# Optimization experiments

Measured on AMD Instinct MI355X. Metric: run time of the kernel, lower is better.

The kernel has to match this reference:

```python
import jax, jax.numpy as jnp
import numpy as np

B, T, I, H, O = 128, 256, 64, 1024, 64


def setup_inputs() -> dict:
    key = jax.random.key(0)
    ks = jax.random.split(key, 16)
    s_ih1 = 1.0 / np.sqrt(H)
    def mk(k, shape, s):
        return jax.random.uniform(k, shape, jnp.float32, -s, s)
    return {
        "x": jax.random.normal(ks[0], (B, T, I), jnp.float32),
        # RNNCell 1: input I -> hidden H
        "W_ih1": mk(ks[1], (H, I), s_ih1),
        "b_ih1": mk(ks[2], (H,), s_ih1),
        "W_hh1": mk(ks[3], (H, H), s_ih1),
        "b_hh1": mk(ks[4], (H,), s_ih1),
        # RNNCell 2: hidden H -> hidden H
        "W_ih2": mk(ks[5], (H, H), s_ih1),
        "b_ih2": mk(ks[6], (H,), s_ih1),
        "W_hh2": mk(ks[7], (H, H), s_ih1),
        "b_hh2": mk(ks[8], (H,), s_ih1),
        # gate: 2H -> H
        "Wg": mk(ks[9], (H, 2 * H), 1.0 / np.sqrt(2 * H)),
        "bg": mk(ks[10], (H,), 1.0 / np.sqrt(2 * H)),
        # output heads: H -> O
        "Wo1": mk(ks[11], (O, H), s_ih1),
        "bo1": mk(ks[12], (O,), s_ih1),
        "Wo2": mk(ks[13], (O, H), s_ih1),
        "bo2": mk(ks[14], (O,), s_ih1),
    }


def reference(x, W_ih1, b_ih1, W_hh1, b_hh1, W_ih2, b_ih2, W_hh2, b_hh2,
              Wg, bg, Wo1, bo1, Wo2, bo2):
    batch = x.shape[0]
    h1_0 = jnp.zeros((batch, H), x.dtype)
    h2_0 = jnp.zeros((batch, H), x.dtype)
    u_0 = jnp.ones((batch, H), x.dtype)

    def step(carry, x_t):
        h1, h2, u = carry
        # RNNCell 1
        h1 = jnp.tanh(x_t @ W_ih1.T + b_ih1 + h1 @ W_hh1.T + b_hh1)
        # RNNCell 2, gated convex blend with previous h2
        h2_new = jnp.tanh(h1 @ W_ih2.T + b_ih2 + h2 @ W_hh2.T + b_hh2)
        h2 = u * h2_new + (1.0 - u) * h2
        # dual tanh output head
        out = jnp.tanh(h1 @ Wo1.T + bo1) + jnp.tanh(h2 @ Wo2.T + bo2)
        # gate for NEXT step, computed from current hiddens
        u = jax.nn.sigmoid(jnp.concatenate([h1, h2], axis=1) @ Wg.T + bg)
        return (h1, h2, u), out

    xs = jnp.swapaxes(x, 0, 1)  # [T, B, I]
    _, outs = jax.lax.scan(step, (h1_0, h2_0, u_0), xs)
    return jnp.swapaxes(outs, 0, 1)  # [B, T, O]
```

## Files before the change

### kernel.cpp

```cpp
#include <hip/hip_runtime.h>
#include <cstddef>

using bf16x8 = __attribute__((ext_vector_type(8))) short;
using f32x4  = __attribute__((ext_vector_type(4))) float;

constexpr int Bb = 128;
constexpr int Tt = 256;
constexpr int Hh = 1024;
constexpr int Oo = 64;
constexpr int NBLK = 200;
constexpr int FLAG_STRIDE = 32;
constexpr int RS = 1048;

constexpr int R_H1 = 8;
constexpr int R_H2 = 16;
constexpr int R_PP = 6;
constexpr int R_PO = 16;

constexpr int FH1 = 0;
constexpr int FP2 = 64;
constexpr int FPG = 96;
constexpr int FPO = 128;
constexpr int FH2 = 160;
constexpr int FZO = 224;

__device__ __forceinline__ float bf2f(short s) {
  unsigned int u = ((unsigned int)(unsigned short)s) << 16;
  float f;
  __builtin_memcpy(&f, &u, 4);
  return f;
}
__device__ __forceinline__ short f2bf(float f) {
  unsigned int u;
  __builtin_memcpy(&u, &f, 4);
  u += 0x7fffu + ((u >> 16) & 1u);
  return (short)(u >> 16);
}
__device__ __forceinline__ bf16x8 as_bf(int4 v) {
  union { int4 i; bf16x8 b; } u; u.i = v; return u.b;
}
__device__ __forceinline__ float ldf(const float* p) {
  return __hip_atomic_load((float*)p, __ATOMIC_RELAXED, __HIP_MEMORY_SCOPE_AGENT);
}
__device__ __forceinline__ void stf(float* p, float v) {
  __hip_atomic_store(p, v, __ATOMIC_RELAXED, __HIP_MEMORY_SCOPE_AGENT);
}
__device__ __forceinline__ unsigned ldu(const unsigned* p) {
  return __hip_atomic_load((unsigned*)p, __ATOMIC_RELAXED, __HIP_MEMORY_SCOPE_AGENT);
}

#define LD16A(d, p) asm volatile("global_load_dwordx4 %0, %1, off sc1" \
                                 : "=v"(d) : "v"((const void*)(p)))

__device__ __forceinline__ void stage_chunk(short* dstAs, const short* src, int tid) {
  const int row = tid >> 3;
  const int c0  = (tid & 7) * 8;
  const short* gp = src + (size_t)row * Hh + c0;
  short* lp = dstAs + row * RS + c0;
  int4 r0[16];
#pragma unroll
  for (int j = 0; j < 16; ++j) LD16A(r0[j], gp + j * 64);
  asm volatile("s_waitcnt vmcnt(0)" ::: "memory");
#pragma unroll
  for (int j = 0; j < 16; ++j) *(int4*)(lp + j * 64) = r0[j];
}

__device__ __forceinline__ void loadW(int4 (&w)[32], const short* B, size_t st,
                                      int lm, int q) {
  const short* bp = B + (size_t)lm * st + q * 8;
#pragma unroll
  for (int c = 0; c < 32; ++c) w[c] = *(const int4*)(bp + c * 32);
}

__device__ __forceinline__ void passW2(const short* As32, int lm, int q,
    const int4 (&w)[32], f32x4& acc0, f32x4& acc1) {
  const short* ap0 = As32 + lm * RS + q * 8;
  const short* ap1 = ap0 + 16 * RS;
#pragma unroll
  for (int c = 0; c < 32; ++c) {
    const bf16x8 a0 = as_bf(*(const int4*)(ap0 + c * 32));
    const bf16x8 a1 = as_bf(*(const int4*)(ap1 + c * 32));
    const bf16x8 b  = as_bf(w[c]);
    acc0 = __builtin_amdgcn_mfma_f32_16x16x32_bf16(a0, b, acc0, 0, 0, 0);
    acc1 = __builtin_amdgcn_mfma_f32_16x16x32_bf16(a1, b, acc1, 0, 0, 0);
  }
}

__device__ __forceinline__ void poll_ge(const unsigned* flags, int base,
                                        int mask, unsigned gen) {
  const unsigned* f = flags + (size_t)(base + (threadIdx.x & mask)) * FLAG_STRIDE;
  while (!__all(ldu(f) >= gen))
    __builtin_amdgcn_s_sleep(2);
}

#define POST_FLAG(SLOT, GEN) do {                                          \
    asm volatile("s_waitcnt vmcnt(0) lgkmcnt(0)" ::: "memory");            \
    __syncthreads();                                                       \
    if (tid == 0)                                                          \
      __hip_atomic_store(p.flags + (size_t)(SLOT) * FLAG_STRIDE,           \
                         (unsigned)(GEN),                                  \
                         __ATOMIC_RELAXED, __HIP_MEMORY_SCOPE_AGENT);      \
  } while (0)

#define ST_BF16_PAIR(BASE, ROW, COL, HV) do {                              \
    const int _ov = __shfl_xor((int)(unsigned short)(HV), 1, 64);          \
    if ((lm & 1) == 0) {                                                   \
      const unsigned _pk = (unsigned)(unsigned short)(HV) | ((unsigned)_ov << 16); \
      __hip_atomic_store((unsigned*)((BASE) + (size_t)(ROW) * Hh + (COL)), _pk, \
                         __ATOMIC_RELAXED, __HIP_MEMORY_SCOPE_AGENT);      \
    } } while (0)

struct RP {
  short *h1ring;
  short *h2ring;
  float *h2f;
  float *pre2f;
  float *pg1f;
  float *po1f;
  const short* prex;
  const short *whh1, *wih2, *whh2, *wg, *wo1, *wo2;
  const float *b_ih2, *b_hh2, *bg, *bo1, *bo2;
  float* out;
  unsigned* flags;
};

__global__ void __launch_bounds__(256, 1) rnn_kernel(RP p) {
  __shared__ short As[64 * RS];
  __shared__ float zbuf[2048];
  const int tid = threadIdx.x;
  const int lane = tid & 63;
  const int wv = tid >> 6;
  const int lm = lane & 15;
  const int q = lane >> 4;
  const int bid = blockIdx.x;

  const size_t HS = (size_t)Bb * Hh;
  const f32x4 z4 = {0.f, 0.f, 0.f, 0.f};
  int4 w[32];

  if (bid < 64) {
    const int g = bid;
    const int mb = (g >> 4) * 32, cb = (g & 15) * 64;
    const int cw = cb + wv * 16;
    loadW(w, p.whh1 + (size_t)cw * Hh, Hh, lm, q);
    for (int t = 0; t < Tt; ++t) {
      short prs[2][4];
      const short* pr = p.prex + (size_t)t * HS;
#pragma unroll
      for (int rf = 0; rf < 2; ++rf)
#pragma unroll
        for (int r = 0; r < 4; ++r)
          prs[rf][r] = pr[(size_t)(mb + rf * 16 + q * 4 + r) * Hh + cw + lm];
      if (tid < 64) {
        if (t >= 1) poll_ge(p.flags, FH1, 63, (unsigned)t);
        if (t >= 8) {
          poll_ge(p.flags, FP2, 31, (unsigned)(t - 7));
          poll_ge(p.flags, FPG, 31, (unsigned)(t - 7));
          poll_ge(p.flags, FPO, 3,  (unsigned)(t - 7));
        }
      }
      __syncthreads();
      const short* h1prev = p.h1ring + (size_t)((t + R_H1 - 1) % R_H1) * HS;
      stage_chunk(As, h1prev + (size_t)mb * Hh, tid);
      __syncthreads();
      f32x4 a0 = z4, a1 = z4;
      passW2(As, lm, q, w, a0, a1);
      short* h1out = p.h1ring + (size_t)(t % R_H1) * HS;
#pragma unroll
      for (int rf = 0; rf < 2; ++rf)
#pragma unroll
        for (int r = 0; r < 4; ++r) {
          const int row = mb + rf * 16 + q * 4 + r;
          const float z = rf ? a1[r] : a0[r];
          const short hv = f2bf(tanhf(z + bf2f(prs[rf][r])));
          ST_BF16_PAIR(h1out, row, cw + lm, hv);
        }
      POST_FLAG(FH1 + g, t + 1);
    }
  } else if (bid < 128) {
    const bool isP2 = (bid < 96);
    const int g = isP2 ? (bid - 64) : (bid - 96);
    const int mb = (g >> 4) * 64, cb = (g & 15) * 64;
    const int cw = cb + wv * 16;
    float bias;
    if (isP2) {
      bias = p.b_ih2[cw + lm] + p.b_hh2[cw + lm];
      loadW(w, p.wih2 + (size_t)cw * Hh, Hh, lm, q);
    } else {
      bias = p.bg[cw + lm];
      loadW(w, p.wg + (size_t)cw * (2 * Hh), 2 * Hh, lm, q);
    }
    const int fbase = isP2 ? FP2 : FPG;
    const int fslot = fbase + g;
    for (int t = 0; t < Tt; ++t) {
      if (tid < 64) {
        poll_ge(p.flags, FH1, 63, (unsigned)(t + 1));
        if (t >= R_PP) poll_ge(p.flags, FH2, 63, (unsigned)(t - (isP2 ? 5 : 4)));
      }
      __syncthreads();
      const short* h1cur = p.h1ring + (size_t)(t % R_H1) * HS;
      stage_chunk(As, h1cur + (size_t)mb * Hh, tid);
      stage_chunk(As + 32 * RS, h1cur + (size_t)(mb + 32) * Hh, tid);
      __syncthreads();
      f32x4 acc[4];
      acc[0] = acc[1] = acc[2] = acc[3] = (f32x4){bias, bias, bias, bias};
      passW2(As, lm, q, w, acc[0], acc[1]);
      passW2(As + 32 * RS, lm, q, w, acc[2], acc[3]);
      float* dst = (isP2 ? p.pre2f : p.pg1f) + (size_t)(t % R_PP) * HS;
#pragma unroll
      for (int rf = 0; rf < 4; ++rf)
#pragma unroll
        for (int r = 0; r < 4; ++r) {
          const int row = mb + rf * 16 + q * 4 + r;
          stf(dst + (size_t)row * Hh + cw + lm, acc[rf][r]);
        }
      POST_FLAG(fslot, t + 1);
    }
  } else if (bid < 192) {
    const int g = bid - 128;
    const int mb = (g >> 5) * 64, cb = (g & 31) * 32;
    const int m = wv >> 1;
    const int ch = wv & 1;
    const int cw = cb + ch * 16;
    if (m == 0) loadW(w, p.whh2 + (size_t)cw * Hh, Hh, lm, q);
    else        loadW(w, p.wg + Hh + (size_t)cw * (2 * Hh), 2 * Hh, lm, q);
    for (int s = 0; s < Tt; ++s) {
      if (tid < 64) {
        poll_ge(p.flags, FP2, 31, (unsigned)(s + 1));
        if (s >= 1) {
          poll_ge(p.flags, FPG, 31, (unsigned)s);
          poll_ge(p.flags, FH2, 63, (unsigned)s);
        }
        if (s >= R_H2) poll_ge(p.flags, FZO, 3, (unsigned)(s - 15));
      }
      __syncthreads();
      float p2v[4][4], pg1v[4][4], hpv[4][4];
      if (m == 0) {
        const float* pre2s = p.pre2f + (size_t)(s % R_PP) * HS;
        const float* pg1s  = p.pg1f + (size_t)((s + R_PP - 1) % R_PP) * HS;
#pragma unroll
        for (int rf = 0; rf < 4; ++rf)
#pragma unroll
          for (int r = 0; r < 4; ++r) {
            const size_t idx = (size_t)(mb + rf * 16 + q * 4 + r) * Hh + cw + lm;
            p2v[rf][r] = ldf(pre2s + idx);
            pg1v[rf][r] = (s > 0) ? ldf(pg1s + idx) : 0.f;
            hpv[rf][r] = p.h2f[idx];
          }
      }
      const short* h2prev = p.h2ring + (size_t)((s + R_H2 - 1) % R_H2) * HS;
      stage_chunk(As, h2prev + (size_t)mb * Hh, tid);
      stage_chunk(As + 32 * RS, h2prev + (size_t)(mb + 32) * Hh, tid);
      __syncthreads();
      f32x4 acc[4];
      acc[0] = acc[1] = acc[2] = acc[3] = z4;
      passW2(As, lm, q, w, acc[0], acc[1]);
      passW2(As + 32 * RS, lm, q, w, acc[2], acc[3]);
      if (m == 1) {
        float* zb = zbuf + ch * 1024;
#pragma unroll
        for (int rf = 0; rf < 4; ++rf)
#pragma unroll
          for (int r = 0; r < 4; ++r)
            zb[(rf * 4 + r) * 64 + lane] = acc[rf][r];
      }
      __syncthreads();
      if (m == 0) {
        const float* zb = zbuf + ch * 1024;
        short* h2out = p.h2ring + (size_t)(s % R_H2) * HS;
#pragma unroll
        for (int rf = 0; rf < 4; ++rf)
#pragma unroll
          for (int r = 0; r < 4; ++r) {
            const int row = mb + rf * 16 + q * 4 + r;
            const size_t idx = (size_t)row * Hh + cw + lm;
            const float zg = zb[(rf * 4 + r) * 64 + lane];
            const float u = (s == 0) ? 1.f
                : 1.f / (1.f + expf(-(zg + pg1v[rf][r])));
            const float hn = tanhf(acc[rf][r] + p2v[rf][r]);
            const float nv = fmaf(u, hn - hpv[rf][r], hpv[rf][r]);
            p.h2f[idx] = nv;
            const short hv = f2bf(nv);
            ST_BF16_PAIR(h2out, row, cw + lm, hv);
          }
      }
      POST_FLAG(FH2 + g, s + 1);
    }
  } else if (bid < 196) {
    const int g = bid - 192;
    const int mb = g * 32;
    const int cw = wv * 16;
    const float bias = p.bo1[cw + lm];
    loadW(w, p.wo1 + (size_t)cw * Hh, Hh, lm, q);
    for (int t = 0; t < Tt; ++t) {
      if (tid < 64) {
        poll_ge(p.flags, FH1, 63, (unsigned)(t + 1));
        if (t >= R_PO) poll_ge(p.flags, FZO, 3, (unsigned)(t - 15));
      }
      __syncthreads();
      const short* h1cur = p.h1ring + (size_t)(t % R_H1) * HS;
      stage_chunk(As, h1cur + (size_t)mb * Hh, tid);
      __syncthreads();
      f32x4 a0 = {bias, bias, bias, bias}, a1 = a0;
      passW2(As, lm, q, w, a0, a1);
      float* dst = p.po1f + (size_t)(t % R_PO) * (Bb * Oo);
#pragma unroll
      for (int rf = 0; rf < 2; ++rf)
#pragma unroll
        for (int r = 0; r < 4; ++r) {
          const int row = mb + rf * 16 + q * 4 + r;
          const float z = rf ? a1[r] : a0[r];
          stf(dst + (size_t)row * Oo + cw + lm, tanhf(z));
        }
      POST_FLAG(FPO + g, t + 1);
    }
  } else {
    const int g = bid - 196;
    const int mb = g * 32;
    const int cw = wv * 16;
    const float bias = p.bo2[cw + lm];
    loadW(w, p.wo2 + (size_t)cw * Hh, Hh, lm, q);
    for (int ot = 0; ot < Tt; ++ot) {
      if (tid < 64) {
        poll_ge(p.flags, FH2, 63, (unsigned)(ot + 1));
        poll_ge(p.flags, FPO, 3,  (unsigned)(ot + 1));
      }
      __syncthreads();
      float pv[2][4];
      const float* po1s = p.po1f + (size_t)(ot % R_PO) * (Bb * Oo);
#pragma unroll
      for (int rf = 0; rf < 2; ++rf)
#pragma unroll
        for (int r = 0; r < 4; ++r)
          pv[rf][r] = ldf(po1s + (size_t)(mb + rf * 16 + q * 4 + r) * Oo + cw + lm);
      const short* h2cur = p.h2ring + (size_t)(ot % R_H2) * HS;
      stage_chunk(As, h2cur + (size_t)mb * Hh, tid);
      __syncthreads();
      f32x4 a0 = {bias, bias, bias, bias}, a1 = a0;
      passW2(As, lm, q, w, a0, a1);
#pragma unroll
      for (int rf = 0; rf < 2; ++rf)
#pragma unroll
        for (int r = 0; r < 4; ++r) {
          const int row = mb + rf * 16 + q * 4 + r;
          const float z = rf ? a1[r] : a0[r];
          p.out[(size_t)row * (Tt * Oo) + (size_t)ot * Oo + cw + lm] =
              pv[rf][r] + tanhf(z);
        }
      POST_FLAG(FZO + g, ot + 1);
    }
  }
}

__global__ void __launch_bounds__(256) prex_kernel(
    const float* __restrict__ x, const float* __restrict__ wih1,
    const float* __restrict__ b_ih1, const float* __restrict__ b_hh1,
    short* __restrict__ prex) {
  const int tid = threadIdx.x;
  const int lane = tid & 63;
  const int wv = tid >> 6;
  const int lm = lane & 15;
  const int q = lane >> 4;
  const int bm = blockIdx.x >> 4;
  const int bn = blockIdx.x & 15;
  const int rowbase = bm * 64;
  const int col = bn * 64 + wv * 16 + lm;

  const f32x4 z4 = {0.f, 0.f, 0.f, 0.f};
  f32x4 acc[4];
#pragma unroll
  for (int mt = 0; mt < 4; ++mt) acc[mt] = z4;

#pragma unroll
  for (int kc = 0; kc < 2; ++kc) {
    const float* bp = wih1 + col * 64 + kc * 32 + q * 8;
    bf16x8 bf;
#pragma unroll
    for (int j = 0; j < 8; ++j) bf[j] = f2bf(bp[j]);
#pragma unroll
    for (int mt = 0; mt < 4; ++mt) {
      const float* ap = x + (size_t)(rowbase + mt * 16 + lm) * 64 + kc * 32 + q * 8;
      bf16x8 af;
#pragma unroll
      for (int j = 0; j < 8; ++j) af[j] = f2bf(ap[j]);
      acc[mt] = __builtin_amdgcn_mfma_f32_16x16x32_bf16(af, bf, acc[mt], 0, 0, 0);
    }
  }
  const float bia = b_ih1[col] + b_hh1[col];
#pragma unroll
  for (int mt = 0; mt < 4; ++mt) {
#pragma unroll
    for (int r = 0; r < 4; ++r) {
      const int row = rowbase + mt * 16 + q * 4 + r;
      const int b  = row >> 8;
      const int tt = row & 255;
      prex[((size_t)tt * Bb + b) * Hh + col] = f2bf(acc[mt][r] + bia);
    }
  }
}

__global__ void conv_kernel(const float* __restrict__ s, short* __restrict__ d, int n) {
  int i = blockIdx.x * blockDim.x + threadIdx.x;
  const int stride = gridDim.x * blockDim.x;
  for (; i < n; i += stride) d[i] = f2bf(s[i]);
}

__global__ void init_kernel(short* h1ring, short* h2ring,
                            float* h2f, unsigned* flags) {
  const int i = blockIdx.x * blockDim.x + threadIdx.x;
  const size_t HS = (size_t)Bb * Hh;
  h1ring[(size_t)(R_H1 - 1) * HS + i] = 0;
  h2ring[(size_t)(R_H2 - 1) * HS + i] = 0;
  h2f[i] = 0.f;
  if (i < 256) flags[i * FLAG_STRIDE] = 0u;
}

extern "C" void kernel_launch(void* const* d_in, const int* in_sizes, int n_in,
                              void* d_out, int out_size, void* d_ws, size_t ws_size,
                              hipStream_t stream) {
  (void)in_sizes; (void)n_in; (void)out_size; (void)ws_size;
  const float* x      = (const float*)d_in[0];
  const float* W_ih1  = (const float*)d_in[1];
  const float* b_ih1  = (const float*)d_in[2];
  const float* W_hh1  = (const float*)d_in[3];
  const float* b_hh1  = (const float*)d_in[4];
  const float* W_ih2  = (const float*)d_in[5];
  const float* b_ih2  = (const float*)d_in[6];
  const float* W_hh2  = (const float*)d_in[7];
  const float* b_hh2  = (const float*)d_in[8];
  const float* Wg     = (const float*)d_in[9];
  const float* bg     = (const float*)d_in[10];
  const float* Wo1    = (const float*)d_in[11];
  const float* bo1    = (const float*)d_in[12];
  const float* Wo2    = (const float*)d_in[13];
  const float* bo2    = (const float*)d_in[14];

  char* ws = (char*)d_ws;
  size_t off = 0;
  auto alloc = [&](size_t bytes) -> void* {
    void* ptr = ws + off;
    off += (bytes + 255) & ~(size_t)255;
    return ptr;
  };
  short* whh1 = (short*)alloc((size_t)Hh * Hh * 2);
  short* wih2 = (short*)alloc((size_t)Hh * Hh * 2);
  short* whh2 = (short*)alloc((size_t)Hh * Hh * 2);
  short* wg   = (short*)alloc((size_t)Hh * 2 * Hh * 2);
  short* wo1  = (short*)alloc((size_t)Oo * Hh * 2);
  short* wo2  = (short*)alloc((size_t)Oo * Hh * 2);
  short* prex = (short*)alloc((size_t)Bb * Tt * Hh * 2);
  short* h1ring = (short*)alloc((size_t)R_H1 * Bb * Hh * 2);
  short* h2ring = (short*)alloc((size_t)R_H2 * Bb * Hh * 2);
  float* h2f  = (float*)alloc((size_t)Bb * Hh * 4);
  float* pre2f= (float*)alloc((size_t)R_PP * Bb * Hh * 4);
  float* pg1f = (float*)alloc((size_t)R_PP * Bb * Hh * 4);
  float* po1f = (float*)alloc((size_t)R_PO * Bb * Oo * 4);
  unsigned* flags = (unsigned*)alloc(256 * FLAG_STRIDE * 4);

  conv_kernel<<<1024, 256, 0, stream>>>(W_hh1, whh1, Hh * Hh);
  conv_kernel<<<1024, 256, 0, stream>>>(W_ih2, wih2, Hh * Hh);
  conv_kernel<<<1024, 256, 0, stream>>>(W_hh2, whh2, Hh * Hh);
  conv_kernel<<<2048, 256, 0, stream>>>(Wg,    wg,   Hh * 2 * Hh);
  conv_kernel<<<256,  256, 0, stream>>>(Wo1,   wo1,  Oo * Hh);
  conv_kernel<<<256,  256, 0, stream>>>(Wo2,   wo2,  Oo * Hh);
  init_kernel<<<512, 256, 0, stream>>>(h1ring, h2ring, h2f, flags);
  prex_kernel<<<8192, 256, 0, stream>>>(x, W_ih1, b_ih1, b_hh1, prex);

  RP p;
  p.h1ring = h1ring; p.h2ring = h2ring;
  p.h2f = h2f; p.pre2f = pre2f; p.pg1f = pg1f; p.po1f = po1f;
  p.prex = prex;
  p.whh1 = whh1; p.wih2 = wih2; p.whh2 = whh2;
  p.wg = wg; p.wo1 = wo1; p.wo2 = wo2;
  p.b_ih2 = b_ih2; p.b_hh2 = b_hh2;
  p.bg = bg; p.bo1 = bo1; p.bo2 = bo2;
  p.out = (float*)d_out;
  p.flags = flags;

  rnn_kernel<<<NBLK, 256, 0, stream>>>(p);
}
```

Measured before the change: 2.692 ms.

## Narrow flag polling to row-group dependencies and defer ring-reuse waits

Each persistent block now polls only the producer flags for the batch-row group it actually reads, instead of waiting on every producer block. Ring-buffer overwrite (WAR) checks move from before staging to just before the output store, so the GEMM work overlaps with slow consumers. The second half of the LDS staging is issued before the first MMA pass and written after it, hiding global load latency. The risks are more __syncthreads per step and correctness that now depends on the exact flag-slot index mapping.

After: 2.743 ms. About the same (+1.9%).

```diff
diff --git a/kernel.cpp b/kernel.cpp
--- a/kernel.cpp
+++ b/kernel.cpp
@@ -52,17 +52,25 @@
 #define LD16A(d, p) asm volatile("global_load_dwordx4 %0, %1, off sc1" \
                                  : "=v"(d) : "v"((const void*)(p)))
 
-__device__ __forceinline__ void stage_chunk(short* dstAs, const short* src, int tid) {
+__device__ __forceinline__ void stage_issue(int4 (&r)[16], const short* src, int tid) {
   const int row = tid >> 3;
   const int c0  = (tid & 7) * 8;
   const short* gp = src + (size_t)row * Hh + c0;
+#pragma unroll
+  for (int j = 0; j < 16; ++j) LD16A(r[j], gp + j * 64);
+}
+__device__ __forceinline__ void stage_write(short* dstAs, int4 (&r)[16], int tid) {
+  const int row = tid >> 3;
+  const int c0  = (tid & 7) * 8;
   short* lp = dstAs + row * RS + c0;
-  int4 r0[16];
-#pragma unroll
-  for (int j = 0; j < 16; ++j) LD16A(r0[j], gp + j * 64);
   asm volatile("s_waitcnt vmcnt(0)" ::: "memory");
 #pragma unroll
-  for (int j = 0; j < 16; ++j) *(int4*)(lp + j * 64) = r0[j];
+  for (int j = 0; j < 16; ++j) *(int4*)(lp + j * 64) = r[j];
+}
+__device__ __forceinline__ void stage_chunk(short* dstAs, const short* src, int tid) {
+  int4 r[16];
+  stage_issue(r, src, tid);
+  stage_write(dstAs, r, tid);
 }
 
 __device__ __forceinline__ void loadW(int4 (&w)[32], const short* B, size_t st,
@@ -140,7 +148,8 @@
 
   if (bid < 64) {
     const int g = bid;
-    const int mb = (g >> 4) * 32, cb = (g & 15) * 64;
+    const int rg = g >> 4;
+    const int mb = rg * 32, cb = (g & 15) * 64;
     const int cw = cb + wv * 16;
     loadW(w, p.whh1 + (size_t)cw * Hh, Hh, lm, q);
     for (int t = 0; t < Tt; ++t) {
@@ -151,20 +160,19 @@
 #pragma unroll
         for (int r = 0; r < 4; ++r)
           prs[rf][r] = pr[(size_t)(mb + rf * 16 + q * 4 + r) * Hh + cw + lm];
-      if (tid < 64) {
-        if (t >= 1) poll_ge(p.flags, FH1, 63, (unsigned)t);
-        if (t >= 8) {
-          poll_ge(p.flags, FP2, 31, (unsigned)(t - 7));
-          poll_ge(p.flags, FPG, 31, (unsigned)(t - 7));
-          poll_ge(p.flags, FPO, 3,  (unsigned)(t - 7));
-        }
-      }
+      if (tid < 64 && t >= 1) poll_ge(p.flags, FH1 + rg * 16, 15, (unsigned)t);
       __syncthreads();
       const short* h1prev = p.h1ring + (size_t)((t + R_H1 - 1) % R_H1) * HS;
       stage_chunk(As, h1prev + (size_t)mb * Hh, tid);
       __syncthreads();
       f32x4 a0 = z4, a1 = z4;
       passW2(As, lm, q, w, a0, a1);
+      if (tid < 64 && t >= 8) {
+        poll_ge(p.flags, FP2 + (rg >> 1) * 16, 15, (unsigned)(t - 7));
+        poll_ge(p.flags, FPG + (rg >> 1) * 16, 15, (unsigned)(t - 7));
+        poll_ge(p.flags, FPO + rg, 0, (unsigned)(t - 7));
+      }
+      __syncthreads();
       short* h1out = p.h1ring + (size_t)(t % R_H1) * HS;
 #pragma unroll
       for (int rf = 0; rf < 2; ++rf)
@@ -180,7 +188,8 @@
   } else if (bid < 128) {
     const bool isP2 = (bid < 96);
     const int g = isP2 ? (bid - 64) : (bid - 96);
-    const int mb = (g >> 4) * 64, cb = (g & 15) * 64;
+    const int rgp = g >> 4, cg = g & 15;
+    const int mb = rgp * 64, cb = cg * 64;
     const int cw = cb + wv * 16;
     float bias;
     if (isP2) {
@@ -190,22 +199,25 @@
       bias = p.bg[cw + lm];
       loadW(w, p.wg + (size_t)cw * (2 * Hh), 2 * Hh, lm, q);
     }
-    const int fbase = isP2 ? FP2 : FPG;
-    const int fslot = fbase + g;
+    const int fslot = (isP2 ? FP2 : FPG) + g;
+    const int gslot = FH2 + rgp * 32 + cg * 2;
+    const int glag = isP2 ? 5 : 4;
     for (int t = 0; t < Tt; ++t) {
-      if (tid < 64) {
-        poll_ge(p.flags, FH1, 63, (unsigned)(t + 1));
-        if (t >= R_PP) poll_ge(p.flags, FH2, 63, (unsigned)(t - (isP2 ? 5 : 4)));
-      }
+      if (tid < 64) poll_ge(p.flags, FH1 + rgp * 32, 31, (unsigned)(t + 1));
       __syncthreads();
       const short* h1cur = p.h1ring + (size_t)(t % R_H1) * HS;
       stage_chunk(As, h1cur + (size_t)mb * Hh, tid);
-      stage_chunk(As + 32 * RS, h1cur + (size_t)(mb + 32) * Hh, tid);
-      __syncthreads();
+      __syncthreads();
+      int4 rB[16];
+      stage_issue(rB, h1cur + (size_t)(mb + 32) * Hh, tid);
       f32x4 acc[4];
       acc[0] = acc[1] = acc[2] = acc[3] = (f32x4){bias, bias, bias, bias};
       passW2(As, lm, q, w, acc[0], acc[1]);
+      stage_write(As + 32 * RS, rB, tid);
+      __syncthreads();
       passW2(As + 32 * RS, lm, q, w, acc[2], acc[3]);
+      if (tid < 64 && t >= R_PP) poll_ge(p.flags, gslot, 1, (unsigned)(t - glag));
+      __syncthreads();
       float* dst = (isP2 ? p.pre2f : p.pg1f) + (size_t)(t % R_PP) * HS;
 #pragma unroll
       for (int rf = 0; rf < 4; ++rf)
@@ -218,21 +230,33 @@
     }
   } else if (bid < 192) {
     const int g = bid - 128;
-    const int mb = (g >> 5) * 64, cb = (g & 31) * 32;
+    const int rgh = g >> 5, cb = (g & 31) * 32;
+    const int mb = rgh * 64;
     const int m = wv >> 1;
     const int ch = wv & 1;
     const int cw = cb + ch * 16;
+    const int fp2slot = FP2 + rgh * 16 + (cb >> 6);
+    const int fpgslot = FPG + rgh * 16 + (cb >> 6);
     if (m == 0) loadW(w, p.whh2 + (size_t)cw * Hh, Hh, lm, q);
     else        loadW(w, p.wg + Hh + (size_t)cw * (2 * Hh), 2 * Hh, lm, q);
     for (int s = 0; s < Tt; ++s) {
       if (tid < 64) {
-        poll_ge(p.flags, FP2, 31, (unsigned)(s + 1));
+        poll_ge(p.flags, fp2slot, 0, (unsigned)(s + 1));
         if (s >= 1) {
-          poll_ge(p.flags, FPG, 31, (unsigned)s);
-          poll_ge(p.flags, FH2, 63, (unsigned)s);
+          poll_ge(p.flags, fpgslot, 0, (unsigned)s);
+          poll_ge(p.flags, FH2 + rgh * 32, 31, (unsigned)s);
         }
-        if (s >= R_H2) poll_ge(p.flags, FZO, 3, (unsigned)(s - 15));
-      }
+      }
+      __syncthreads();
+      const short* h2prev = p.h2ring + (size_t)((s + R_H2 - 1) % R_H2) * HS;
+      stage_chunk(As, h2prev + (size_t)mb * Hh, tid);
+      __syncthreads();
+      int4 rB[16];
+      stage_issue(rB, h2prev + (size_t)(mb + 32) * Hh, tid);
+      f32x4 acc[4];
+      acc[0] = acc[1] = acc[2] = acc[3] = z4;
+      passW2(As, lm, q, w, acc[0], acc[1]);
+      stage_write(As + 32 * RS, rB, tid);
       __syncthreads();
       float p2v[4][4], pg1v[4][4], hpv[4][4];
       if (m == 0) {
@@ -248,13 +272,6 @@
             hpv[rf][r] = p.h2f[idx];
           }
       }
-      const short* h2prev = p.h2ring + (size_t)((s + R_H2 - 1) % R_H2) * HS;
-      stage_chunk(As, h2prev + (size_t)mb * Hh, tid);
-      stage_chunk(As + 32 * RS, h2prev + (size_t)(mb + 32) * Hh, tid);
-      __syncthreads();
-      f32x4 acc[4];
-      acc[0] = acc[1] = acc[2] = acc[3] = z4;
-      passW2(As, lm, q, w, acc[0], acc[1]);
       passW2(As + 32 * RS, lm, q, w, acc[2], acc[3]);
       if (m == 1) {
         float* zb = zbuf + ch * 1024;
@@ -264,6 +281,7 @@
           for (int r = 0; r < 4; ++r)
             zb[(rf * 4 + r) * 64 + lane] = acc[rf][r];
       }
+      if (tid < 64 && s >= R_H2) poll_ge(p.flags, FZO + rgh * 2, 1, (unsigned)(s - 15));
       __syncthreads();
       if (m == 0) {
         const float* zb = zbuf + ch * 1024;
@@ -293,16 +311,15 @@
     const float bias = p.bo1[cw + lm];
     loadW(w, p.wo1 + (size_t)cw * Hh, Hh, lm, q);
     for (int t = 0; t < Tt; ++t) {
-      if (tid < 64) {
-        poll_ge(p.flags, FH1, 63, (unsigned)(t + 1));
-        if (t >= R_PO) poll_ge(p.flags, FZO, 3, (unsigned)(t - 15));
-      }
+      if (tid < 64) poll_ge(p.flags, FH1 + g * 16, 15, (unsigned)(t + 1));
       __syncthreads();
       const short* h1cur = p.h1ring + (size_t)(t % R_H1) * HS;
       stage_chunk(As, h1cur + (size_t)mb * Hh, tid);
       __syncthreads();
       f32x4 a0 = {bias, bias, bias, bias}, a1 = a0;
       passW2(As, lm, q, w, a0, a1);
+      if (tid < 64 && t >= R_PO) poll_ge(p.flags, FZO + g, 0, (unsigned)(t - 15));
+      __syncthreads();
       float* dst = p.po1f + (size_t)(t % R_PO) * (Bb * Oo);
 #pragma unroll
       for (int rf = 0; rf < 2; ++rf)
@@ -322,8 +339,8 @@
     loadW(w, p.wo2 + (size_t)cw * Hh, Hh, lm, q);
     for (int ot = 0; ot < Tt; ++ot) {
       if (tid < 64) {
-        poll_ge(p.flags, FH2, 63, (unsigned)(ot + 1));
-        poll_ge(p.flags, FPO, 3,  (unsigned)(ot + 1));
+        poll_ge(p.flags, FH2 + (g >> 1) * 32, 31, (unsigned)(ot + 1));
+        poll_ge(p.flags, FPO + g, 0, (unsigned)(ot + 1));
       }
       __syncthreads();
       float pv[2][4];
```
